# Kernel optimization log

Hardware: AMD Instinct MI355X
Metric: run time of the kernel (lower is better)

The kernel has to match this reference:

```python
import jax, jax.numpy as jnp
import numpy as np

B, T, C, L = 256, 512, 128, 64  # batch, timesteps, num_classes (blank=C-1), max label len
NEG = -1e30  # finite -inf surrogate (avoids nan in grads)


def setup_inputs() -> dict:
    key = jax.random.key(0)
    k1, k2, k3, k4 = jax.random.split(key, 4)
    logits = jax.random.normal(k1, (B, T, C), dtype=jnp.float32)
    y_pred = jax.nn.softmax(logits, axis=-1)  # ctc_batch_cost expects softmax probs
    y_true = jax.random.randint(k2, (B, L), 0, C - 1, dtype=jnp.int32)  # non-blank labels
    input_length = jax.random.randint(k3, (B, 1), T // 2, T + 1, dtype=jnp.int32)
    label_length = jax.random.randint(k4, (B, 1), L // 2, L + 1, dtype=jnp.int32)
    return {"y_true": y_true, "y_pred": y_pred,
            "input_length": input_length, "label_length": label_length}


def _ctc_loss(log_probs, labels, input_length, label_length, blank):
    # log_probs: [B,T,C]; labels: [B,L]; lengths: [B]
    b, t_max, _ = log_probs.shape
    l_max = labels.shape[1]
    s_max = 2 * l_max + 1
    # extended label sequence: blank, l1, blank, l2, ..., blank  -> [B,S]
    ext = jnp.full((b, s_max), blank, dtype=labels.dtype)
    ext = ext.at[:, 1::2].set(labels)
    # gathered log probs per extended symbol: [B,T,S]
    lp = jnp.take_along_axis(log_probs, ext[:, None, :].astype(jnp.int32), axis=2)
    # skip (s-2 -> s) allowed where ext[s] != blank and ext[s] != ext[s-2]
    skip = jnp.zeros((b, s_max), dtype=bool)
    skip = skip.at[:, 2:].set((ext[:, 2:] != blank) & (ext[:, 2:] != ext[:, :-2]))
    # init alpha at t=0: only s=0 (blank) and s=1 (first label) reachable
    alpha0 = jnp.full((b, s_max), NEG, dtype=log_probs.dtype)
    alpha0 = alpha0.at[:, 0].set(lp[:, 0, 0])
    alpha0 = alpha0.at[:, 1].set(lp[:, 0, 1])
    in_len = input_length

    def step(alpha, inp):
        lp_t, t = inp  # lp_t: [B,S]
        s1 = jnp.pad(alpha, ((0, 0), (1, 0)), constant_values=NEG)[:, :-1]
        s2 = jnp.pad(alpha, ((0, 0), (2, 0)), constant_values=NEG)[:, :-2]
        a = jnp.logaddexp(alpha, s1)
        a = jnp.where(skip, jnp.logaddexp(a, s2), a)
        new = a + lp_t
        new = jnp.where((t < in_len)[:, None], new, alpha)  # freeze past input_length
        return new, None

    lp_time_major = jnp.swapaxes(lp, 0, 1)  # [T,B,S]
    ts = jnp.arange(1, t_max)
    alpha, _ = jax.lax.scan(step, alpha0, (lp_time_major[1:], ts))
    lab = label_length
    idx_last = 2 * lab  # final blank position; idx_last-1 is final label position
    a_last = jnp.take_along_axis(alpha, idx_last[:, None], axis=1)[:, 0]
    a_prev = jnp.take_along_axis(alpha, (idx_last - 1)[:, None], axis=1)[:, 0]
    return -jnp.logaddexp(a_last, a_prev)  # [B]


def reference(y_true, y_pred, input_length, label_length):
    eps = 1e-7  # keras epsilon added before log
    log_probs = jnp.log(y_pred + eps)
    blank = y_pred.shape[-1] - 1  # keras ctc_batch_cost blank convention
    loss = _ctc_loss(log_probs, y_true, input_length[:, 0], label_length[:, 0], blank)
    return loss[:, None]  # [B,1], matching tf expand_dims(ctc_loss, 1)
```

## Files before the change

### kernel.cpp

```cpp
#include <hip/hip_runtime.h>


#define B_ 256
#define T_ 512
#define C_ 128
#define L_ 64
#define BLANK_ 127
#define EPSF (1e-7f)
#define CHUNK 32
#define QSTR 36
#define LN2F 0.6931471805599453f

#define EXP2(x) __builtin_amdgcn_exp2f(x)
#define LOG2(x) __builtin_amdgcn_logf(x)

__device__ __forceinline__ float lse2_2(float a, float b) {
    float m = fmaxf(a, b);
    float d = fminf(a, b) - m;
    return m + LOG2(1.0f + EXP2(d));
}

__device__ __forceinline__ float dppf(float x) {
    return __int_as_float(__builtin_amdgcn_update_dpp(
        0, __float_as_int(x), 0x138, 0xf, 0xf, false));
}
__device__ __forceinline__ int dppi(int x) {
    return __builtin_amdgcn_update_dpp(0, x, 0x138, 0xf, 0xf, false);
}

__device__ __forceinline__ void stage_chunk(const float* gsrc, float* ldst, int lane) {
#pragma unroll
    for (int i = 0; i < CHUNK / 2; ++i) {
        __builtin_amdgcn_global_load_lds(
            (const __attribute__((address_space(1))) void*)(gsrc + i * 256 + lane * 4),
            (__attribute__((address_space(3))) void*)(ldst + i * 256),
            16, 0, 0);
    }
}

__device__ __forceinline__ void produce_chunk(const float* __restrict__ rk,
        float* __restrict__ qd, int lane, int label, int t0, int tend, float& llg)
{
    const float pbv = rk[(lane & 31) * C_ + BLANK_] + EPSF;
    const float rpb = 0.5f / pbv;
    const int t = t0 + lane;
    const bool lgv = (lane < 32) && (t >= 1) && (t < tend);
    llg += lgv ? LOG2(pbv) : 0.0f;
#pragma unroll
    for (int k = 0; k < 8; ++k) {
        float q[4];
#pragma unroll
        for (int j = 0; j < 4; ++j) {
            const int r = 4 * k + j;
            const float pl = rk[r * C_ + label] + EPSF;
            const float rb = __int_as_float(
                __builtin_amdgcn_readlane(__float_as_int(rpb), r));
            q[j] = pl * rb;
        }
        *reinterpret_cast<float4*>(qd + lane * QSTR + 4 * k) =
            make_float4(q[0], q[1], q[2], q[3]);
    }
}

template<bool HAS128>
__device__ __forceinline__ void maybe_renorm(float& A0, float& A1, float& A2,
                                             int& e, float& sch, float& kq,
                                             float skipf2) {
    float m2 = fmaxf(A0, A1);
    if (HAS128) m2 = fmaxf(m2, A2);
    const bool out = (m2 > 16777216.0f) ||
                     ((m2 < 5.9604644775390625e-8f) && (m2 > 0.0f));
    if (__any(out)) {
        const float mm = (m2 == 0.0f) ? 1.0f : m2;
        const int eb = __float_as_int(mm) >> 23;
        const float s = __int_as_float((254 - eb) << 23);
        A0 *= s; A1 *= s;
        if (HAS128) A2 *= s;
        e += eb - 127;
        const int ep = dppi(e);
        int d = ep - e;
        d = d < -125 ? -125 : d;
        d = d > 127 ? 127 : d;
        sch = __int_as_float((d + 126) << 23);
        kq = skipf2 * sch;
    }
}

template<bool HAS128>
__device__ __forceinline__ void step(float& A0, float& A1, float& A2,
                                     float sch, float kq, float ql) {
    const float s1 = dppf(A1);
    const float Y  = A1 + A0;
    const float A2n = HAS128 ? (A2 + A1) * 0.5f : A2;
    const float P1 = s1 * sch;
    const float A1n = fmaf(kq, s1, Y) * ql;
    const float A0n = fmaf(A0, 0.5f, P1);
    A0 = A0n; A1 = A1n;
    if (HAS128) A2 = A2n;
}

template<bool HAS128>
__device__ __forceinline__ void consumer(const float (*qlbuf)[64 * QSTR],
        const float* extra, int lane, int label, int lab, int tend, int nmax,
        float* out, int b)
{
    const int lprev = __shfl_up(label, 1);
    const float skipf2 = (lane > 0 && label != lprev) ? 2.0f : 0.0f;

    float A0 = 0.0f, A1 = 0.0f, A2 = 0.0f;
    float sch = 0.5f, kq = skipf2 * 0.5f;
    int e = 0;

    for (int c = 0; c < nmax; ++c) {
        const float* qb = &qlbuf[c & 1][lane * QSTR];
        float qlv[32];
#pragma unroll
        for (int k = 0; k < 8; ++k) {
            const float4 t4 = *reinterpret_cast<const float4*>(qb + 4 * k);
            qlv[4*k+0] = t4.x; qlv[4*k+1] = t4.y;
            qlv[4*k+2] = t4.z; qlv[4*k+3] = t4.w;
        }
        asm volatile("s_waitcnt lgkmcnt(0)" ::: "memory");
        __builtin_amdgcn_s_barrier();
        __builtin_amdgcn_sched_barrier(0);

        const int rem = tend - c * CHUNK;
        if (c == 0) {
            A0 = (lane == 0) ? extra[1] : 0.0f;
            A1 = (lane == 0) ? extra[0] : 0.0f;
#pragma unroll
            for (int u = 1; u < 32; ++u) {
                step<HAS128>(A0, A1, A2, sch, kq, qlv[u]);
                if ((u & 3) == 3)
                    maybe_renorm<HAS128>(A0, A1, A2, e, sch, kq, skipf2);
            }
        } else if (rem >= CHUNK) {
#pragma unroll
            for (int u = 0; u < 32; ++u) {
                step<HAS128>(A0, A1, A2, sch, kq, qlv[u]);
                if ((u & 3) == 3)
                    maybe_renorm<HAS128>(A0, A1, A2, e, sch, kq, skipf2);
            }
        } else {
            for (int u = 0; u < rem; ++u) {
                step<HAS128>(A0, A1, A2, sch, kq, qlv[u]);
                if ((u & 3) == 3)
                    maybe_renorm<HAS128>(A0, A1, A2, e, sch, kq, skipf2);
            }
        }
    }
    __builtin_amdgcn_s_barrier();
    const float lg = extra[2];
    const float ef = (float)e + lg + (float)(tend - 1);
    const float l0 = LOG2(A0) + ef;
    const float l1 = LOG2(A1) + ef;
    const float a_prev = __shfl(l1, lab - 1);
    float a_last;
    if (HAS128) {
        const float l2 = LOG2(A2) + ef;
        a_last = __shfl(l2, 63);
    } else {
        a_last = __shfl(l0, lab);
    }
    if (lane == 0) out[b] = -LN2F * lse2_2(a_last, a_prev);
}

__global__ __launch_bounds__(128) void ctc_fwd_kernel(
    const int* __restrict__ y_true, const float* __restrict__ y_pred,
    const int* __restrict__ input_len, const int* __restrict__ label_len,
    float* __restrict__ out)
{
    __shared__ __align__(16) float raw[2][CHUNK * C_];
    __shared__ __align__(16) float qlbuf[2][64 * QSTR];
    __shared__ float extra[4];

    const int b = blockIdx.x;
    const int tid = threadIdx.x;
    const int lane = tid & 63;
    const float* __restrict__ Pg = y_pred + (size_t)b * T_ * C_;
    const int label = y_true[b * L_ + lane];
    const int in_len = input_len[b];
    const int tend = in_len < T_ ? in_len : T_;
    const int nmax = (tend + CHUNK - 1) / CHUNK;

    if (tid >= 64) {
        float llg = 0.0f;
        stage_chunk(Pg, &raw[0][0], lane);
        stage_chunk(Pg + CHUNK * C_, &raw[1][0], lane);
        asm volatile("s_waitcnt vmcnt(16)" ::: "memory");
        produce_chunk(&raw[0][0], &qlbuf[0][0], lane, label, 0, tend, llg);
        if (lane == 0) {
            extra[0] = raw[0][label] + EPSF;
            extra[1] = raw[0][BLANK_] + EPSF;
        }
        asm volatile("s_waitcnt lgkmcnt(0)" ::: "memory");
        __builtin_amdgcn_s_barrier();
        for (int c = 0; c < nmax; ++c) {
            if (c + 2 < nmax)
                stage_chunk(Pg + (size_t)(c + 2) * CHUNK * C_, &raw[c & 1][0], lane);
            if (c + 1 < nmax) {
                if (c + 2 < nmax) asm volatile("s_waitcnt vmcnt(16)" ::: "memory");
                else              asm volatile("s_waitcnt vmcnt(0)" ::: "memory");
                produce_chunk(&raw[(c + 1) & 1][0], &qlbuf[(c + 1) & 1][0],
                              lane, label, (c + 1) * CHUNK, tend, llg);
            }
            asm volatile("s_waitcnt lgkmcnt(0)" ::: "memory");
            __builtin_amdgcn_s_barrier();
        }
#pragma unroll
        for (int off = 16; off >= 1; off >>= 1) llg += __shfl_xor(llg, off);
        if (lane == 0) extra[2] = llg;
        asm volatile("s_waitcnt lgkmcnt(0)" ::: "memory");
        __builtin_amdgcn_s_barrier();
    } else {
        const int lab = label_len[b];
        __builtin_amdgcn_s_barrier();
        if (lab == L_) consumer<true >(qlbuf, extra, lane, label, lab, tend, nmax, out, b);
        else           consumer<false>(qlbuf, extra, lane, label, lab, tend, nmax, out, b);
    }
}

extern "C" void kernel_launch(void* const* d_in, const int* in_sizes, int n_in,
                              void* d_out, int out_size, void* d_ws, size_t ws_size,
                              hipStream_t stream) {
    const int*   y_true    = (const int*)d_in[0];
    const float* y_pred    = (const float*)d_in[1];
    const int*   input_len = (const int*)d_in[2];
    const int*   label_len = (const int*)d_in[3];
    float* out = (float*)d_out;

    ctc_fwd_kernel<<<B_, 128, 0, stream>>>(y_true, y_pred, input_len, label_len, out);
}
```

Baseline: 25.90 us.

## Deepen producer/consumer pipeline with triple-buffered LDS and register prefetch

The producer now keeps four raw chunks of global-to-LDS loads in flight and runs two chunks ahead into a triple-buffered q buffer. The consumer prefetches the next chunk's q values into registers while computing the current chunk, which takes the LDS read latency off the serial recurrence. The q layout moves from a padded per-lane row to a time-major [r*64+lane] layout, giving conflict-free scalar LDS access. The cost is more LDS use, 64 live registers for q, and a more complex vmcnt schedule.

```diff
diff --git a/kernel.cpp b/kernel.cpp
--- a/kernel.cpp
+++ b/kernel.cpp
@@ -8,7 +8,6 @@
 #define BLANK_ 127
 #define EPSF (1e-7f)
 #define CHUNK 32
-#define QSTR 36
 #define LN2F 0.6931471805599453f
 
 #define EXP2(x) __builtin_amdgcn_exp2f(x)
@@ -46,19 +45,13 @@
     const int t = t0 + lane;
     const bool lgv = (lane < 32) && (t >= 1) && (t < tend);
     llg += lgv ? LOG2(pbv) : 0.0f;
-#pragma unroll
-    for (int k = 0; k < 8; ++k) {
-        float q[4];
-#pragma unroll
-        for (int j = 0; j < 4; ++j) {
-            const int r = 4 * k + j;
-            const float pl = rk[r * C_ + label] + EPSF;
-            const float rb = __int_as_float(
-                __builtin_amdgcn_readlane(__float_as_int(rpb), r));
-            q[j] = pl * rb;
-        }
-        *reinterpret_cast<float4*>(qd + lane * QSTR + 4 * k) =
-            make_float4(q[0], q[1], q[2], q[3]);
+    float* qb = qd + lane;
+#pragma unroll
+    for (int r = 0; r < CHUNK; ++r) {
+        const float pl = rk[r * C_ + label] + EPSF;
+        const float rb = __int_as_float(
+            __builtin_amdgcn_readlane(__float_as_int(rpb), r));
+        qb[r * 64] = pl * rb;
     }
 }
 
@@ -100,78 +93,83 @@
 }
 
 template<bool HAS128>
-__device__ __forceinline__ void consumer(const float (*qlbuf)[64 * QSTR],
-        const float* extra, int lane, int label, int lab, int tend, int nmax,
-        float* out, int b)
-{
-    const int lprev = __shfl_up(label, 1);
-    const float skipf2 = (lane > 0 && label != lprev) ? 2.0f : 0.0f;
-
-    float A0 = 0.0f, A1 = 0.0f, A2 = 0.0f;
-    float sch = 0.5f, kq = skipf2 * 0.5f;
-    int e = 0;
-
-    for (int c = 0; c < nmax; ++c) {
-        const float* qb = &qlbuf[c & 1][lane * QSTR];
-        float qlv[32];
-#pragma unroll
-        for (int k = 0; k < 8; ++k) {
-            const float4 t4 = *reinterpret_cast<const float4*>(qb + 4 * k);
-            qlv[4*k+0] = t4.x; qlv[4*k+1] = t4.y;
-            qlv[4*k+2] = t4.z; qlv[4*k+3] = t4.w;
-        }
-        asm volatile("s_waitcnt lgkmcnt(0)" ::: "memory");
-        __builtin_amdgcn_s_barrier();
+struct Consumer {
+    const float (*qlb)[CHUNK * 64];
+    const float* extra;
+    int lane, lab, tend, nmax, b;
+    float* out;
+    float A0, A1, A2, sch, kq, skipf2;
+    int e;
+
+    __device__ __forceinline__ void loadq(int c, float* arr) {
+        const float* qb = &qlb[c % 3][lane];
+#pragma unroll
+        for (int r = 0; r < CHUNK; ++r) arr[r] = qb[r * 64];
+    }
+
+    __device__ __forceinline__ void iter(int c, float* cur, float* nxt) {
+        if (c + 1 < nmax) loadq(c + 1, nxt);
         __builtin_amdgcn_sched_barrier(0);
-
         const int rem = tend - c * CHUNK;
         if (c == 0) {
             A0 = (lane == 0) ? extra[1] : 0.0f;
             A1 = (lane == 0) ? extra[0] : 0.0f;
 #pragma unroll
             for (int u = 1; u < 32; ++u) {
-                step<HAS128>(A0, A1, A2, sch, kq, qlv[u]);
+                step<HAS128>(A0, A1, A2, sch, kq, cur[u]);
                 if ((u & 3) == 3)
                     maybe_renorm<HAS128>(A0, A1, A2, e, sch, kq, skipf2);
             }
         } else if (rem >= CHUNK) {
 #pragma unroll
             for (int u = 0; u < 32; ++u) {
-                step<HAS128>(A0, A1, A2, sch, kq, qlv[u]);
+                step<HAS128>(A0, A1, A2, sch, kq, cur[u]);
                 if ((u & 3) == 3)
                     maybe_renorm<HAS128>(A0, A1, A2, e, sch, kq, skipf2);
             }
         } else {
             for (int u = 0; u < rem; ++u) {
-                step<HAS128>(A0, A1, A2, sch, kq, qlv[u]);
+                step<HAS128>(A0, A1, A2, sch, kq, cur[u]);
                 if ((u & 3) == 3)
                     maybe_renorm<HAS128>(A0, A1, A2, e, sch, kq, skipf2);
             }
         }
-    }
-    __builtin_amdgcn_s_barrier();
-    const float lg = extra[2];
-    const float ef = (float)e + lg + (float)(tend - 1);
-    const float l0 = LOG2(A0) + ef;
-    const float l1 = LOG2(A1) + ef;
-    const float a_prev = __shfl(l1, lab - 1);
-    float a_last;
-    if (HAS128) {
-        const float l2 = LOG2(A2) + ef;
-        a_last = __shfl(l2, 63);
-    } else {
-        a_last = __shfl(l0, lab);
-    }
-    if (lane == 0) out[b] = -LN2F * lse2_2(a_last, a_prev);
-}
+        asm volatile("s_waitcnt lgkmcnt(0)" ::: "memory");
+        __builtin_amdgcn_s_barrier();
+    }
+
+    __device__ __forceinline__ void run() {
+        float qA[CHUNK], qB[CHUNK];
+        loadq(0, qA);
+        int c = 0;
+        for (;;) {
+            iter(c, qA, qB); if (++c >= nmax) break;
+            iter(c, qB, qA); if (++c >= nmax) break;
+        }
+        __builtin_amdgcn_s_barrier();
+        const float lg = extra[2];
+        const float ef = (float)e + lg + (float)(tend - 1);
+        const float l0 = LOG2(A0) + ef;
+        const float l1 = LOG2(A1) + ef;
+        const float a_prev = __shfl(l1, lab - 1);
+        float a_last;
+        if (HAS128) {
+            const float l2 = LOG2(A2) + ef;
+            a_last = __shfl(l2, 63);
+        } else {
+            a_last = __shfl(l0, lab);
+        }
+        if (lane == 0) out[b] = -LN2F * lse2_2(a_last, a_prev);
+    }
+};
 
 __global__ __launch_bounds__(128) void ctc_fwd_kernel(
     const int* __restrict__ y_true, const float* __restrict__ y_pred,
     const int* __restrict__ input_len, const int* __restrict__ label_len,
     float* __restrict__ out)
 {
-    __shared__ __align__(16) float raw[2][CHUNK * C_];
-    __shared__ __align__(16) float qlbuf[2][64 * QSTR];
+    __shared__ __align__(16) float raw[4][CHUNK * C_];
+    __shared__ __align__(16) float qlb[3][CHUNK * 64];
     __shared__ float extra[4];
 
     const int b = blockIdx.x;
@@ -185,24 +183,32 @@
 
     if (tid >= 64) {
         float llg = 0.0f;
-        stage_chunk(Pg, &raw[0][0], lane);
-        stage_chunk(Pg + CHUNK * C_, &raw[1][0], lane);
-        asm volatile("s_waitcnt vmcnt(16)" ::: "memory");
-        produce_chunk(&raw[0][0], &qlbuf[0][0], lane, label, 0, tend, llg);
+#pragma unroll
+        for (int k = 0; k < 4; ++k)
+            stage_chunk(Pg + (size_t)k * CHUNK * C_, &raw[k][0], lane);
+        asm volatile("s_waitcnt vmcnt(48)" ::: "memory");
+        produce_chunk(&raw[0][0], &qlb[0][0], lane, label, 0, tend, llg);
         if (lane == 0) {
             extra[0] = raw[0][label] + EPSF;
             extra[1] = raw[0][BLANK_] + EPSF;
         }
+        asm volatile("s_waitcnt vmcnt(32)" ::: "memory");
+        produce_chunk(&raw[1][0], &qlb[1][0], lane, label, CHUNK, tend, llg);
         asm volatile("s_waitcnt lgkmcnt(0)" ::: "memory");
         __builtin_amdgcn_s_barrier();
-        for (int c = 0; c < nmax; ++c) {
-            if (c + 2 < nmax)
-                stage_chunk(Pg + (size_t)(c + 2) * CHUNK * C_, &raw[c & 1][0], lane);
-            if (c + 1 < nmax) {
-                if (c + 2 < nmax) asm volatile("s_waitcnt vmcnt(16)" ::: "memory");
-                else              asm volatile("s_waitcnt vmcnt(0)" ::: "memory");
-                produce_chunk(&raw[(c + 1) & 1][0], &qlbuf[(c + 1) & 1][0],
-                              lane, label, (c + 1) * CHUNK, tend, llg);
+        for (int i = 0; i < nmax; ++i) {
+            if (i + 4 < nmax)
+                stage_chunk(Pg + (size_t)(i + 4) * CHUNK * C_,
+                            &raw[(i + 4) & 3][0], lane);
+            if (i + 2 < nmax) {
+                if (i + 4 < nmax)
+                    asm volatile("s_waitcnt vmcnt(32)" ::: "memory");
+                else if (i + 3 < nmax)
+                    asm volatile("s_waitcnt vmcnt(16)" ::: "memory");
+                else
+                    asm volatile("s_waitcnt vmcnt(0)" ::: "memory");
+                produce_chunk(&raw[(i + 2) & 3][0], &qlb[(i + 2) % 3][0],
+                              lane, label, (i + 2) * CHUNK, tend, llg);
             }
             asm volatile("s_waitcnt lgkmcnt(0)" ::: "memory");
             __builtin_amdgcn_s_barrier();
@@ -213,10 +219,19 @@
         asm volatile("s_waitcnt lgkmcnt(0)" ::: "memory");
         __builtin_amdgcn_s_barrier();
     } else {
+        const int lprev = __shfl_up(label, 1);
+        const float skipf2 = (lane > 0 && label != lprev) ? 2.0f : 0.0f;
         const int lab = label_len[b];
         __builtin_amdgcn_s_barrier();
-        if (lab == L_) consumer<true >(qlbuf, extra, lane, label, lab, tend, nmax, out, b);
-        else           consumer<false>(qlbuf, extra, lane, label, lab, tend, nmax, out, b);
+        if (lab == L_) {
+            Consumer<true> cns{qlb, extra, lane, lab, tend, nmax, b, out,
+                               0.0f, 0.0f, 0.0f, 0.5f, skipf2 * 0.5f, skipf2, 0};
+            cns.run();
+        } else {
+            Consumer<false> cns{qlb, extra, lane, lab, tend, nmax, b, out,
+                                0.0f, 0.0f, 0.0f, 0.5f, skipf2 * 0.5f, skipf2, 0};
+            cns.run();
+        }
     }
 }
 
```

Result: slower. 36.00 us (+39.0%).

## Split producer work across three waves with four-deep q-buffer ring

Applied to the files above, without the earlier changes.

Grows the block from two waves to four: three producer waves each own every third chunk, with their own double-buffered raw staging, and write into a four-slot ring of q buffers. The consumer wave now reads its chunk values after the barrier of the previous iteration and puts one barrier at the end of each chunk. The q layout changes from lane-major with padding to time-major, so the consumer reads conflict-free scalar LDS values. The goal is to take the producer and global-load latency off the consumer's serial recurrence. The cost is a larger LDS footprint, more waves per block, and a per-chunk barrier that still ties all waves together.

```diff
diff --git a/kernel.cpp b/kernel.cpp
--- a/kernel.cpp
+++ b/kernel.cpp
@@ -8,7 +8,6 @@
 #define BLANK_ 127
 #define EPSF (1e-7f)
 #define CHUNK 32
-#define QSTR 36
 #define LN2F 0.6931471805599453f
 
 #define EXP2(x) __builtin_amdgcn_exp2f(x)
@@ -46,19 +45,13 @@
     const int t = t0 + lane;
     const bool lgv = (lane < 32) && (t >= 1) && (t < tend);
     llg += lgv ? LOG2(pbv) : 0.0f;
-#pragma unroll
-    for (int k = 0; k < 8; ++k) {
-        float q[4];
-#pragma unroll
-        for (int j = 0; j < 4; ++j) {
-            const int r = 4 * k + j;
-            const float pl = rk[r * C_ + label] + EPSF;
-            const float rb = __int_as_float(
-                __builtin_amdgcn_readlane(__float_as_int(rpb), r));
-            q[j] = pl * rb;
-        }
-        *reinterpret_cast<float4*>(qd + lane * QSTR + 4 * k) =
-            make_float4(q[0], q[1], q[2], q[3]);
+    float* qb = qd + lane;
+#pragma unroll
+    for (int r = 0; r < CHUNK; ++r) {
+        const float pl = rk[r * C_ + label] + EPSF;
+        const float rb = __int_as_float(
+            __builtin_amdgcn_readlane(__float_as_int(rpb), r));
+        qb[r * 64] = pl * rb;
     }
 }
 
@@ -100,28 +93,19 @@
 }
 
 template<bool HAS128>
-__device__ __forceinline__ void consumer(const float (*qlbuf)[64 * QSTR],
-        const float* extra, int lane, int label, int lab, int tend, int nmax,
-        float* out, int b)
+__device__ __forceinline__ void consumer_run(const float (*qlb)[CHUNK * 64],
+        const float* extra, int lane, int lab, int tend, int nmax,
+        float skipf2, float* out, int b)
 {
-    const int lprev = __shfl_up(label, 1);
-    const float skipf2 = (lane > 0 && label != lprev) ? 2.0f : 0.0f;
-
     float A0 = 0.0f, A1 = 0.0f, A2 = 0.0f;
     float sch = 0.5f, kq = skipf2 * 0.5f;
     int e = 0;
 
     for (int c = 0; c < nmax; ++c) {
-        const float* qb = &qlbuf[c & 1][lane * QSTR];
-        float qlv[32];
-#pragma unroll
-        for (int k = 0; k < 8; ++k) {
-            const float4 t4 = *reinterpret_cast<const float4*>(qb + 4 * k);
-            qlv[4*k+0] = t4.x; qlv[4*k+1] = t4.y;
-            qlv[4*k+2] = t4.z; qlv[4*k+3] = t4.w;
-        }
-        asm volatile("s_waitcnt lgkmcnt(0)" ::: "memory");
-        __builtin_amdgcn_s_barrier();
+        const float* qb = &qlb[c & 3][lane];
+        float q[CHUNK];
+#pragma unroll
+        for (int r = 0; r < CHUNK; ++r) q[r] = qb[r * 64];
         __builtin_amdgcn_sched_barrier(0);
 
         const int rem = tend - c * CHUNK;
@@ -130,27 +114,28 @@
             A1 = (lane == 0) ? extra[0] : 0.0f;
 #pragma unroll
             for (int u = 1; u < 32; ++u) {
-                step<HAS128>(A0, A1, A2, sch, kq, qlv[u]);
+                step<HAS128>(A0, A1, A2, sch, kq, q[u]);
                 if ((u & 3) == 3)
                     maybe_renorm<HAS128>(A0, A1, A2, e, sch, kq, skipf2);
             }
         } else if (rem >= CHUNK) {
 #pragma unroll
             for (int u = 0; u < 32; ++u) {
-                step<HAS128>(A0, A1, A2, sch, kq, qlv[u]);
+                step<HAS128>(A0, A1, A2, sch, kq, q[u]);
                 if ((u & 3) == 3)
                     maybe_renorm<HAS128>(A0, A1, A2, e, sch, kq, skipf2);
             }
         } else {
             for (int u = 0; u < rem; ++u) {
-                step<HAS128>(A0, A1, A2, sch, kq, qlv[u]);
+                step<HAS128>(A0, A1, A2, sch, kq, q[u]);
                 if ((u & 3) == 3)
                     maybe_renorm<HAS128>(A0, A1, A2, e, sch, kq, skipf2);
             }
         }
+        __builtin_amdgcn_s_barrier();
     }
     __builtin_amdgcn_s_barrier();
-    const float lg = extra[2];
+    const float lg = extra[2] + extra[3] + extra[4];
     const float ef = (float)e + lg + (float)(tend - 1);
     const float l0 = LOG2(A0) + ef;
     const float l1 = LOG2(A1) + ef;
@@ -165,58 +150,69 @@
     if (lane == 0) out[b] = -LN2F * lse2_2(a_last, a_prev);
 }
 
-__global__ __launch_bounds__(128) void ctc_fwd_kernel(
+__global__ __launch_bounds__(256) void ctc_fwd_kernel(
     const int* __restrict__ y_true, const float* __restrict__ y_pred,
     const int* __restrict__ input_len, const int* __restrict__ label_len,
     float* __restrict__ out)
 {
-    __shared__ __align__(16) float raw[2][CHUNK * C_];
-    __shared__ __align__(16) float qlbuf[2][64 * QSTR];
-    __shared__ float extra[4];
+    __shared__ __align__(16) float raw[3][2][CHUNK * C_];
+    __shared__ __align__(16) float qlb[4][CHUNK * 64];
+    __shared__ float extra[8];
 
     const int b = blockIdx.x;
     const int tid = threadIdx.x;
     const int lane = tid & 63;
+    const int wid = tid >> 6;
     const float* __restrict__ Pg = y_pred + (size_t)b * T_ * C_;
     const int label = y_true[b * L_ + lane];
     const int in_len = input_len[b];
     const int tend = in_len < T_ ? in_len : T_;
     const int nmax = (tend + CHUNK - 1) / CHUNK;
 
-    if (tid >= 64) {
+    if (wid > 0) {
+        const int pi = wid - 1;
         float llg = 0.0f;
-        stage_chunk(Pg, &raw[0][0], lane);
-        stage_chunk(Pg + CHUNK * C_, &raw[1][0], lane);
+        stage_chunk(Pg + (size_t)pi * CHUNK * C_, &raw[pi][0][0], lane);
+        stage_chunk(Pg + (size_t)(pi + 3) * CHUNK * C_, &raw[pi][1][0], lane);
         asm volatile("s_waitcnt vmcnt(16)" ::: "memory");
-        produce_chunk(&raw[0][0], &qlbuf[0][0], lane, label, 0, tend, llg);
-        if (lane == 0) {
-            extra[0] = raw[0][label] + EPSF;
-            extra[1] = raw[0][BLANK_] + EPSF;
+        produce_chunk(&raw[pi][0][0], &qlb[pi][0], lane, label,
+                      pi * CHUNK, tend, llg);
+        if (pi == 0 && lane == 0) {
+            extra[0] = raw[0][0][label]  + EPSF;
+            extra[1] = raw[0][0][BLANK_] + EPSF;
         }
         asm volatile("s_waitcnt lgkmcnt(0)" ::: "memory");
         __builtin_amdgcn_s_barrier();
-        for (int c = 0; c < nmax; ++c) {
-            if (c + 2 < nmax)
-                stage_chunk(Pg + (size_t)(c + 2) * CHUNK * C_, &raw[c & 1][0], lane);
-            if (c + 1 < nmax) {
-                if (c + 2 < nmax) asm volatile("s_waitcnt vmcnt(16)" ::: "memory");
-                else              asm volatile("s_waitcnt vmcnt(0)" ::: "memory");
-                produce_chunk(&raw[(c + 1) & 1][0], &qlbuf[(c + 1) & 1][0],
-                              lane, label, (c + 1) * CHUNK, tend, llg);
-            }
-            asm volatile("s_waitcnt lgkmcnt(0)" ::: "memory");
+        for (int i = 0; i < nmax; ++i) {
+            if (i % 3 == pi) {
+                const int js = i + 6, jp = i + 3;
+                if (js < nmax)
+                    stage_chunk(Pg + (size_t)js * CHUNK * C_,
+                                &raw[pi][(js / 3) & 1][0], lane);
+                if (jp < nmax) {
+                    if (js < nmax) asm volatile("s_waitcnt vmcnt(16)" ::: "memory");
+                    else           asm volatile("s_waitcnt vmcnt(0)" ::: "memory");
+                    produce_chunk(&raw[pi][(jp / 3) & 1][0], &qlb[jp & 3][0],
+                                  lane, label, jp * CHUNK, tend, llg);
+                    asm volatile("s_waitcnt lgkmcnt(0)" ::: "memory");
+                }
+            }
             __builtin_amdgcn_s_barrier();
         }
 #pragma unroll
         for (int off = 16; off >= 1; off >>= 1) llg += __shfl_xor(llg, off);
-        if (lane == 0) extra[2] = llg;
+        if (lane == 0) extra[2 + pi] = llg;
         asm volatile("s_waitcnt lgkmcnt(0)" ::: "memory");
         __builtin_amdgcn_s_barrier();
     } else {
+        const int lprev = __shfl_up(label, 1);
+        const float skipf2 = (lane > 0 && label != lprev) ? 2.0f : 0.0f;
         const int lab = label_len[b];
         __builtin_amdgcn_s_barrier();
-        if (lab == L_) consumer<true >(qlbuf, extra, lane, label, lab, tend, nmax, out, b);
-        else           consumer<false>(qlbuf, extra, lane, label, lab, tend, nmax, out, b);
+        if (lab == L_)
+            consumer_run<true >(qlb, extra, lane, lab, tend, nmax, skipf2, out, b);
+        else
+            consumer_run<false>(qlb, extra, lane, lab, tend, nmax, skipf2, out, b);
     }
 }
 
@@ -229,5 +225,5 @@
     const int*   label_len = (const int*)d_in[3];
     float* out = (float*)d_out;
 
-    ctc_fwd_kernel<<<B_, 128, 0, stream>>>(y_true, y_pred, input_len, label_len, out);
-}
+    ctc_fwd_kernel<<<B_, 256, 0, stream>>>(y_true, y_pred, input_len, label_len, out);
+}
```

After: 35.69 us. 1.38x slower.

## Double consumer step size to 64 timesteps per barrier and predicate tail

Applied to the files above, without the earlier changes.

Producer now stages and converts two 32-row chunks per iteration into a 64-wide per-lane buffer, so the consumer synchronises once per 64 timesteps instead of 32. The consumer's barrier moves after its compute, and the partial final block is fully unrolled with select-based masking instead of a dynamic loop. The reciprocal of the blank probability uses the hardware rcp instruction. This trades fewer barriers for more LDS, more registers, and wasted steps in the masked tail.

```diff
diff --git a/kernel.cpp b/kernel.cpp
--- a/kernel.cpp
+++ b/kernel.cpp
@@ -8,7 +8,8 @@
 #define BLANK_ 127
 #define EPSF (1e-7f)
 #define CHUNK 32
-#define QSTR 36
+#define ISTEP 64
+#define QSTR 68
 #define LN2F 0.6931471805599453f
 
 #define EXP2(x) __builtin_amdgcn_exp2f(x)
@@ -42,7 +43,7 @@
         float* __restrict__ qd, int lane, int label, int t0, int tend, float& llg)
 {
     const float pbv = rk[(lane & 31) * C_ + BLANK_] + EPSF;
-    const float rpb = 0.5f / pbv;
+    const float rpb = __builtin_amdgcn_rcpf(pbv) * 0.5f;
     const int t = t0 + lane;
     const bool lgv = (lane < 32) && (t >= 1) && (t < tend);
     llg += lgv ? LOG2(pbv) : 0.0f;
@@ -57,7 +58,7 @@
                 __builtin_amdgcn_readlane(__float_as_int(rpb), r));
             q[j] = pl * rb;
         }
-        *reinterpret_cast<float4*>(qd + lane * QSTR + 4 * k) =
+        *reinterpret_cast<float4*>(qd + 4 * k) =
             make_float4(q[0], q[1], q[2], q[3]);
     }
 }
@@ -100,54 +101,55 @@
 }
 
 template<bool HAS128>
-__device__ __forceinline__ void consumer(const float (*qlbuf)[64 * QSTR],
-        const float* extra, int lane, int label, int lab, int tend, int nmax,
-        float* out, int b)
+__device__ __forceinline__ void consumer_run(const float (*qlb)[64 * QSTR],
+        const float* extra, int lane, int lab, int tend, int nI,
+        float skipf2, float* out, int b)
 {
-    const int lprev = __shfl_up(label, 1);
-    const float skipf2 = (lane > 0 && label != lprev) ? 2.0f : 0.0f;
-
     float A0 = 0.0f, A1 = 0.0f, A2 = 0.0f;
     float sch = 0.5f, kq = skipf2 * 0.5f;
     int e = 0;
 
-    for (int c = 0; c < nmax; ++c) {
-        const float* qb = &qlbuf[c & 1][lane * QSTR];
-        float qlv[32];
-#pragma unroll
-        for (int k = 0; k < 8; ++k) {
+    for (int c = 0; c < nI; ++c) {
+        const float* qb = &qlb[c & 1][lane * QSTR];
+        float q[ISTEP];
+#pragma unroll
+        for (int k = 0; k < ISTEP / 4; ++k) {
             const float4 t4 = *reinterpret_cast<const float4*>(qb + 4 * k);
-            qlv[4*k+0] = t4.x; qlv[4*k+1] = t4.y;
-            qlv[4*k+2] = t4.z; qlv[4*k+3] = t4.w;
-        }
-        asm volatile("s_waitcnt lgkmcnt(0)" ::: "memory");
-        __builtin_amdgcn_s_barrier();
+            q[4*k+0] = t4.x; q[4*k+1] = t4.y;
+            q[4*k+2] = t4.z; q[4*k+3] = t4.w;
+        }
         __builtin_amdgcn_sched_barrier(0);
 
-        const int rem = tend - c * CHUNK;
+        const int rem = tend - c * ISTEP;
         if (c == 0) {
             A0 = (lane == 0) ? extra[1] : 0.0f;
             A1 = (lane == 0) ? extra[0] : 0.0f;
 #pragma unroll
-            for (int u = 1; u < 32; ++u) {
-                step<HAS128>(A0, A1, A2, sch, kq, qlv[u]);
+            for (int u = 1; u < ISTEP; ++u) {
+                step<HAS128>(A0, A1, A2, sch, kq, q[u]);
                 if ((u & 3) == 3)
                     maybe_renorm<HAS128>(A0, A1, A2, e, sch, kq, skipf2);
             }
-        } else if (rem >= CHUNK) {
-#pragma unroll
-            for (int u = 0; u < 32; ++u) {
-                step<HAS128>(A0, A1, A2, sch, kq, qlv[u]);
+        } else if (rem >= ISTEP) {
+#pragma unroll
+            for (int u = 0; u < ISTEP; ++u) {
+                step<HAS128>(A0, A1, A2, sch, kq, q[u]);
                 if ((u & 3) == 3)
                     maybe_renorm<HAS128>(A0, A1, A2, e, sch, kq, skipf2);
             }
         } else {
-            for (int u = 0; u < rem; ++u) {
-                step<HAS128>(A0, A1, A2, sch, kq, qlv[u]);
+#pragma unroll
+            for (int u = 0; u < ISTEP; ++u) {
+                const float A0o = A0, A1o = A1, A2o = A2;
+                step<HAS128>(A0, A1, A2, sch, kq, q[u]);
+                const bool v = u < rem;
+                A0 = v ? A0 : A0o; A1 = v ? A1 : A1o;
+                if (HAS128) A2 = v ? A2 : A2o;
                 if ((u & 3) == 3)
                     maybe_renorm<HAS128>(A0, A1, A2, e, sch, kq, skipf2);
             }
         }
+        __builtin_amdgcn_s_barrier();
     }
     __builtin_amdgcn_s_barrier();
     const float lg = extra[2];
@@ -170,8 +172,8 @@
     const int* __restrict__ input_len, const int* __restrict__ label_len,
     float* __restrict__ out)
 {
-    __shared__ __align__(16) float raw[2][CHUNK * C_];
-    __shared__ __align__(16) float qlbuf[2][64 * QSTR];
+    __shared__ __align__(16) float raw[2][ISTEP * C_];
+    __shared__ __align__(16) float qlb[2][64 * QSTR];
     __shared__ float extra[4];
 
     const int b = blockIdx.x;
@@ -181,30 +183,42 @@
     const int label = y_true[b * L_ + lane];
     const int in_len = input_len[b];
     const int tend = in_len < T_ ? in_len : T_;
-    const int nmax = (tend + CHUNK - 1) / CHUNK;
+    const int nI = (tend + ISTEP - 1) / ISTEP;
 
     if (tid >= 64) {
         float llg = 0.0f;
         stage_chunk(Pg, &raw[0][0], lane);
-        stage_chunk(Pg + CHUNK * C_, &raw[1][0], lane);
-        asm volatile("s_waitcnt vmcnt(16)" ::: "memory");
-        produce_chunk(&raw[0][0], &qlbuf[0][0], lane, label, 0, tend, llg);
+        stage_chunk(Pg + CHUNK * C_, &raw[0][CHUNK * C_], lane);
+        stage_chunk(Pg + (size_t)ISTEP * C_, &raw[1][0], lane);
+        stage_chunk(Pg + (size_t)(ISTEP + CHUNK) * C_, &raw[1][CHUNK * C_], lane);
+        asm volatile("s_waitcnt vmcnt(32)" ::: "memory");
+        produce_chunk(&raw[0][0], &qlb[0][lane * QSTR], lane, label,
+                      0, tend, llg);
+        produce_chunk(&raw[0][CHUNK * C_], &qlb[0][lane * QSTR + CHUNK],
+                      lane, label, CHUNK, tend, llg);
         if (lane == 0) {
-            extra[0] = raw[0][label] + EPSF;
+            extra[0] = raw[0][label]  + EPSF;
             extra[1] = raw[0][BLANK_] + EPSF;
         }
         asm volatile("s_waitcnt lgkmcnt(0)" ::: "memory");
         __builtin_amdgcn_s_barrier();
-        for (int c = 0; c < nmax; ++c) {
-            if (c + 2 < nmax)
-                stage_chunk(Pg + (size_t)(c + 2) * CHUNK * C_, &raw[c & 1][0], lane);
-            if (c + 1 < nmax) {
-                if (c + 2 < nmax) asm volatile("s_waitcnt vmcnt(16)" ::: "memory");
-                else              asm volatile("s_waitcnt vmcnt(0)" ::: "memory");
-                produce_chunk(&raw[(c + 1) & 1][0], &qlbuf[(c + 1) & 1][0],
-                              lane, label, (c + 1) * CHUNK, tend, llg);
-            }
-            asm volatile("s_waitcnt lgkmcnt(0)" ::: "memory");
+        for (int i = 0; i < nI; ++i) {
+            const int js = i + 2, jp = i + 1;
+            if (js < nI) {
+                stage_chunk(Pg + (size_t)js * ISTEP * C_, &raw[js & 1][0], lane);
+                stage_chunk(Pg + ((size_t)js * ISTEP + CHUNK) * C_,
+                            &raw[js & 1][CHUNK * C_], lane);
+            }
+            if (jp < nI) {
+                if (js < nI) asm volatile("s_waitcnt vmcnt(32)" ::: "memory");
+                else         asm volatile("s_waitcnt vmcnt(0)" ::: "memory");
+                produce_chunk(&raw[jp & 1][0], &qlb[jp & 1][lane * QSTR],
+                              lane, label, jp * ISTEP, tend, llg);
+                produce_chunk(&raw[jp & 1][CHUNK * C_],
+                              &qlb[jp & 1][lane * QSTR + CHUNK],
+                              lane, label, jp * ISTEP + CHUNK, tend, llg);
+                asm volatile("s_waitcnt lgkmcnt(0)" ::: "memory");
+            }
             __builtin_amdgcn_s_barrier();
         }
 #pragma unroll
@@ -213,10 +227,14 @@
         asm volatile("s_waitcnt lgkmcnt(0)" ::: "memory");
         __builtin_amdgcn_s_barrier();
     } else {
+        const int lprev = __shfl_up(label, 1);
+        const float skipf2 = (lane > 0 && label != lprev) ? 2.0f : 0.0f;
         const int lab = label_len[b];
         __builtin_amdgcn_s_barrier();
-        if (lab == L_) consumer<true >(qlbuf, extra, lane, label, lab, tend, nmax, out, b);
-        else           consumer<false>(qlbuf, extra, lane, label, lab, tend, nmax, out, b);
+        if (lab == L_)
+            consumer_run<true >(qlb, extra, lane, lab, tend, nI, skipf2, out, b);
+        else
+            consumer_run<false>(qlb, extra, lane, lab, tend, nI, skipf2, out, b);
     }
 }
 
```

After: 25.66 us. Within noise of the previous version (-1.0%).
